# Kernel tuning notes

Hardware: AMD Instinct MI355X
Metric: run time of the kernel (lower is better)

## Reference

```python
import jax, jax.numpy as jnp
import numpy as np

# Problem dimensions (see shape_source)
N_TOTAL = 2048   # canonical nodes in batch
M = 8            # subgraphs per canonical node
K = 16           # sampled nodes per subgraph
S = N_TOTAL * M  # 16384 subgraphs
F = S * K        # 262144 flat nodes
E = 1048576      # intra-subgraph edges (64 per subgraph)
G = 128          # graphs in batch
D = 64           # hidden_dim
H = 4            # num_heads
DH = D // H
MAX_DIST = 32
NUM_LAYERS = 4
IN_CH = 119
EDGE_DIM = 5


def setup_inputs() -> dict:
    key = jax.random.key(0)
    ks = jax.random.split(key, 24)
    x_idx = jax.random.randint(ks[0], (F,), 0, IN_CH)
    edge_attr_idx = jax.random.randint(ks[1], (E,), 1, EDGE_DIM + 1)  # bond labels 1..5 (code does -1)
    # edges stay inside their subgraph: 64 edges per subgraph
    eps = E // S
    sub_of_edge = jnp.arange(E) // eps
    src = sub_of_edge * K + jax.random.randint(ks[2], (E,), 0, K)
    dst = sub_of_edge * K + jax.random.randint(ks[3], (E,), 0, K)
    node_ids = jax.random.randint(ks[4], (F,), 0, N_TOTAL)
    drop = jax.random.uniform(ks[5], (F,)) < 0.1
    is_root = (jnp.arange(F) % K) == 0
    node_ids = jnp.where(drop & (~is_root), -1, node_ids)
    node_ids = jnp.where(is_root, jnp.arange(F) // (K * M), node_ids)
    lp = -3.0 * jax.random.uniform(ks[6], (S,))  # log sampling probs (finite, negative)
    batch = jnp.sort(jax.random.randint(ks[7], (N_TOTAL,), 0, G))
    s = 0.02
    atom_emb = s * jax.random.normal(ks[8], (IN_CH, D))
    bond_emb = s * jax.random.normal(ks[9], (EDGE_DIM, D))
    dist_emb = s * jax.random.normal(ks[10], (MAX_DIST + 1, D))
    logp_w = s * jax.random.normal(ks[11], (1, D))
    logp_b = jnp.zeros((D,))
    mlp_w1 = s * jax.random.normal(ks[12], (NUM_LAYERS, D, D))
    mlp_b1 = jnp.zeros((NUM_LAYERS, D))
    mlp_w2 = s * jax.random.normal(ks[13], (NUM_LAYERS, D, D))
    mlp_b2 = jnp.zeros((NUM_LAYERS, D))
    ht_alpha = jnp.ones((1,))
    in_proj_w = s * jax.random.normal(ks[14], (3 * D, D))
    in_proj_b = jnp.zeros((3 * D,))
    out_proj_w = s * jax.random.normal(ks[15], (D, D))
    out_proj_b = jnp.zeros((D,))
    bn_gamma = jnp.ones((D,))
    bn_beta = jnp.zeros((D,))
    return {
        'x_idx': x_idx, 'edge_attr_idx': edge_attr_idx, 'src': src, 'dst': dst,
        'node_ids': node_ids, 'lp': lp, 'batch': batch,
        'atom_emb': atom_emb, 'bond_emb': bond_emb, 'dist_emb': dist_emb,
        'logp_w': logp_w, 'logp_b': logp_b,
        'mlp_w1': mlp_w1, 'mlp_b1': mlp_b1, 'mlp_w2': mlp_w2, 'mlp_b2': mlp_b2,
        'ht_alpha': ht_alpha, 'in_proj_w': in_proj_w, 'in_proj_b': in_proj_b,
        'out_proj_w': out_proj_w, 'out_proj_b': out_proj_b,
        'bn_gamma': bn_gamma, 'bn_beta': bn_beta,
    }


def reference(x_idx, edge_attr_idx, src, dst, node_ids, lp, batch,
              atom_emb, bond_emb, dist_emb, logp_w, logp_b,
              mlp_w1, mlp_b1, mlp_w2, mlp_b2, ht_alpha,
              in_proj_w, in_proj_b, out_proj_w, out_proj_b,
              bn_gamma, bn_beta):
    # --- embed nodes / bonds ---
    x_flat = atom_emb[x_idx]                       # [F, D]
    ea = bond_emb[edge_attr_idx - 1]               # [E, D]
    sub_batch = jnp.arange(F) // K                 # flat node -> subgraph id
    root = jnp.arange(S) * K
    # --- BFS distances from each subgraph root (edge relaxation, MAX_DIST iters) ---
    big = jnp.int32(MAX_DIST + K)
    d0 = jnp.full((F,), big, dtype=jnp.int32).at[root].set(0)
    def bfs_step(d, _):
        return d.at[dst].min(d[src] + 1), None
    dist, _ = jax.lax.scan(bfs_step, d0, None, length=MAX_DIST)
    dist = jnp.minimum(dist, MAX_DIST)
    dist_pe = dist_emb[dist]                       # [F, D]
    # --- log-prob positional encoding ---
    lp_s = jnp.where(jnp.isfinite(lp), lp, 0.0)    # [S]
    logp_pe = jax.nn.relu(lp_s[sub_batch][:, None] * logp_w[0][None, :] + logp_b)
    valid = node_ids >= 0
    vf = valid[:, None].astype(x_flat.dtype)
    h = (x_flat + dist_pe + logp_pe) * vf          # [F, D]
    # --- GINE-style message passing layers (Arch9Layer assumed: sum-aggregate ReLU(h_src+e) -> 2-layer MLP, residual, validity mask) ---
    for l in range(NUM_LAYERS):
        msg = jax.nn.relu(h[src] + ea)             # [E, D]
        agg = jax.ops.segment_sum(msg, dst, num_segments=F)
        z = jax.nn.relu(agg @ mlp_w1[l] + mlp_b1[l]) @ mlp_w2[l] + mlp_b2[l]
        h = (h + z) * vf
    # --- per-subgraph sum readout ---
    h_sub = jax.ops.segment_sum(h * vf, sub_batch, num_segments=S)  # [S, D]
    h3 = h_sub.reshape(N_TOTAL, M, D)
    # --- HT-biased multihead attention over the m subgraphs of each node ---
    bias = (-ht_alpha[0] * lp_s.reshape(N_TOTAL, M))[:, None, None, :]  # key-only bias [N,1,1,m]
    qkv = h3 @ in_proj_w.T + in_proj_b
    q, k_, v = jnp.split(qkv, 3, axis=-1)
    q = q.reshape(N_TOTAL, M, H, DH)
    k_ = k_.reshape(N_TOTAL, M, H, DH)
    v = v.reshape(N_TOTAL, M, H, DH)
    scores = jnp.einsum('nqhd,nkhd->nhqk', q, k_) / np.sqrt(DH).astype(np.float32) + bias
    attn = jax.nn.softmax(scores, axis=-1)
    o = jnp.einsum('nhqk,nkhd->nqhd', attn, v).reshape(N_TOTAL, M, D)
    o = o @ out_proj_w.T + out_proj_b
    h_attn = o + h3
    # --- mean over subgraphs, batchnorm (training-mode batch stats), graph pooling ---
    pooled = h_attn.mean(axis=1)                   # [N_TOTAL, D]
    mu = pooled.mean(axis=0)
    var = pooled.var(axis=0)
    node_emb = (pooled - mu) / jnp.sqrt(var + 1e-5) * bn_gamma + bn_beta
    return jax.ops.segment_sum(node_emb, batch, num_segments=G)   # [G, D]
```

## Files before the change

kernel.cpp:

```cpp
#include <hip/hip_runtime.h>
#include <hip/hip_bf16.h>

typedef __hip_bfloat16 bf16;
typedef __attribute__((ext_vector_type(8))) short bf16x8;
typedef __attribute__((ext_vector_type(4))) float f32x4;
typedef __attribute__((ext_vector_type(4))) unsigned u32x4;

#define N_TOTAL 2048
#define M_SUB   8
#define KN      16
#define S_SUB   16384
#define F_NODES 262144
#define E_EDGES 1048576
#define G_GRAPHS 128
#define D_DIM   64
#define EPS_SUB 64

#define H_ROWB  272
#define B_ROWB  272

__device__ __forceinline__ float b2f(bf16 x) { return __bfloat162float(x); }
__device__ __forceinline__ float bfu2f(unsigned short u) {
    return __uint_as_float(((unsigned)u) << 16);
}

__device__ __forceinline__ bool get_isbf(const void* alpha) {
    return ((const unsigned short*)alpha)[0] == 0x3F80;
}
__device__ __forceinline__ float ldf(const void* p, int i, bool isbf) {
    if (isbf) return __bfloat162float(((const bf16*)p)[i]);
    return ((const float*)p)[i];
}
__device__ __forceinline__ unsigned f2bf(float x) {
    return (unsigned)__builtin_bit_cast(unsigned short, __float2bfloat16(x));
}
__device__ __forceinline__ unsigned cvt_pk_bf16(float a, float b) {
    unsigned r;
    asm("v_cvt_pk_bf16_f32 %0, %1, %2" : "=v"(r) : "v"(a), "v"(b));
    return r;
}

__global__ __launch_bounds__(256) void k_prew(
    const void* __restrict__ mlp_w1, const void* __restrict__ mlp_w2,
    const void* __restrict__ alpha_p, unsigned short* __restrict__ wb)
{
    const bool isbf = get_isbf(alpha_p);
    int t = blockIdx.x * 256 + threadIdx.x;
    int L   = t >> 13;
    int rem = t & 8191;
    int mi  = rem >> 12;
    int wdx = rem & 4095;
    int row = wdx >> 6, col = wdx & 63;
    int kb = row >> 5, c = col >> 4;
    int f  = kb * 4 + c;
    int lane_ = (((row >> 3) & 3) << 4) | (col & 15);
    int u  = row & 7;
    float val = ldf(mi ? mlp_w2 : mlp_w1, L * 4096 + wdx, isbf);
    wb[((((L * 2 + mi) * 8 + f) * 64 + lane_) << 3) + u] = (unsigned short)f2bf(val);
}

__global__ __launch_bounds__(256) void k_subgraph(
    const int* __restrict__ x_idx, const int* __restrict__ eattr,
    const int* __restrict__ src, const int* __restrict__ dst,
    const int* __restrict__ node_ids, const void* __restrict__ lp,
    const void* __restrict__ atom_emb, const void* __restrict__ bond_emb,
    const void* __restrict__ dist_emb, const void* __restrict__ logp_w,
    const void* __restrict__ logp_b,
    const void* __restrict__ mlp_b1, const void* __restrict__ mlp_b2,
    const void* __restrict__ alpha_p,
    const unsigned short* __restrict__ wbg,
    float* __restrict__ hsub)
{
    __shared__ __align__(16) float sh_h[4][KN][68];
    __shared__ __align__(16) unsigned short ab_bf[4][KN*72];
    __shared__ __align__(16) float sh_bond[5 * 68];
    __shared__ int   sh_im[4][16];
    __shared__ int   sh_dist[4][16];
    __shared__ float sh_vf[4][16];
    __shared__ int   sh_xi[4][16];

    const int tid = threadIdx.x;
    const int w   = tid >> 6;
    const int j   = tid & 63;
    const int s   = blockIdx.x * 4 + w;
    const int q   = j & 15, g = j >> 4;
    const bool isbf = get_isbf(alpha_p);

    if (isbf) {
        const bf16* bp = (const bf16*)bond_emb;
        for (int t = tid; t < 5 * 64; t += 256) {
            int a = t >> 6, ch = t & 63;
            sh_bond[a * 68 + (ch & 15) * 4 + (ch >> 4)] = b2f(bp[t]);
        }
    } else {
        const float* bp = (const float*)bond_emb;
        for (int t = tid; t < 5 * 64; t += 256) {
            int a = t >> 6, ch = t & 63;
            sh_bond[a * 68 + (ch & 15) * 4 + (ch >> 4)] = bp[t];
        }
    }

    int eidx = s * EPS_SUB + j;
    int esrc = src[eidx]  - s * KN;
    int edst = dst[eidx]  - s * KN;
    int ea   = eattr[eidx] - 1;

    if (j < KN) {
        int f = s * KN + j;
        sh_xi[w][j]  = x_idx[f];
        sh_vf[w][j]  = (node_ids[f] >= 0) ? 1.0f : 0.0f;
        sh_im[w][j]  = 0;
    }
    __syncthreads();

    atomicOr(&sh_im[w][edst], 1 << esrc);

    unsigned pk = (unsigned)(esrc * H_ROWB) | ((unsigned)edst << 12)
                | ((unsigned)(ea * B_ROWB) << 16);
    const unsigned qq16 = (unsigned)(q * 16) * 0x00010001u;
    unsigned d0[8], d1[8];
    u32x4 ic0, ic1;
    #pragma unroll
    for (int up = 0; up < 4; ++up) {
        unsigned pa = (unsigned)__shfl((int)pk, 8 * g + 2 * up);
        unsigned pb = (unsigned)__shfl((int)pk, 8 * g + 2 * up + 1);
        unsigned pc = (unsigned)__shfl((int)pk, 32 + 8 * g + 2 * up);
        unsigned pd = (unsigned)__shfl((int)pk, 32 + 8 * g + 2 * up + 1);
        d0[2*up]   = (pa & 0xFFFF0FFFu) + qq16;
        d0[2*up+1] = (pb & 0xFFFF0FFFu) + qq16;
        d1[2*up]   = (pc & 0xFFFF0FFFu) + qq16;
        d1[2*up+1] = (pd & 0xFFFF0FFFu) + qq16;
        ic0[up] = ((((pa >> 12) & 15u) == (unsigned)q) ? 0x3F80u : 0u)
                | ((((pb >> 12) & 15u) == (unsigned)q) ? 0x3F800000u : 0u);
        ic1[up] = ((((pc >> 12) & 15u) == (unsigned)q) ? 0x3F80u : 0u)
                | ((((pd >> 12) & 15u) == (unsigned)q) ? 0x3F800000u : 0u);
    }
    const bf16x8 incf0 = __builtin_bit_cast(bf16x8, ic0);
    const bf16x8 incf1 = __builtin_bit_cast(bf16x8, ic1);

    {
        int inm  = (j < 16) ? sh_im[w][j] : 0;
        int dist = (j == 0) ? 0 : 48;
        unsigned reached = 1u;
        #pragma unroll
        for (int t = 1; t < 16; ++t) {
            bool r = (inm & (int)reached) != 0;
            unsigned long long b = __ballot(r);
            if (r && dist == 48) dist = t;
            reached |= (unsigned)(b & 0xFFFFu);
        }
        if (j < 16) sh_dist[w][j] = dist;
    }

    float vfr[4]; int xi4[4], di4[4];
    #pragma unroll
    for (int r = 0; r < 4; ++r) {
        int n = 4 * g + r;
        vfr[r] = sh_vf[w][n];
        xi4[r] = sh_xi[w][n];
        int d  = sh_dist[w][n];
        di4[r] = d > 32 ? 32 : d;
    }

    char* const hbase = (char*)&sh_h[w][0][0];
    const char* const bondb = (const char*)sh_bond;

    float hreg[4][4];
    {
        const float lp_s = ldf(lp, s, isbf);
        if (isbf) {
            const bf16* wp = (const bf16*)logp_w;
            const bf16* bp = (const bf16*)logp_b;
            const bf16* ap = (const bf16*)atom_emb;
            const bf16* dp = (const bf16*)dist_emb;
            #pragma unroll
            for (int c = 0; c < 4; ++c) {
                int ch = c * 16 + q;
                float lpe = fmaxf(lp_s * b2f(wp[ch]) + b2f(bp[ch]), 0.0f);
                #pragma unroll
                for (int r = 0; r < 4; ++r)
                    hreg[c][r] = (b2f(ap[xi4[r] * 64 + ch]) + b2f(dp[di4[r] * 64 + ch]) + lpe) * vfr[r];
            }
        } else {
            const float* wp = (const float*)logp_w;
            const float* bp = (const float*)logp_b;
            const float* ap = (const float*)atom_emb;
            const float* dp = (const float*)dist_emb;
            #pragma unroll
            for (int c = 0; c < 4; ++c) {
                int ch = c * 16 + q;
                float lpe = fmaxf(lp_s * wp[ch] + bp[ch], 0.0f);
                #pragma unroll
                for (int r = 0; r < 4; ++r)
                    hreg[c][r] = (ap[xi4[r] * 64 + ch] + dp[di4[r] * 64 + ch] + lpe) * vfr[r];
            }
        }
        #pragma unroll
        for (int r = 0; r < 4; ++r) {
            float4 v = {hreg[0][r], hreg[1][r], hreg[2][r], hreg[3][r]};
            *(float4*)(hbase + (4 * g + r) * H_ROWB + q * 16) = v;
        }
    }

    const bf16x8* wbv = (const bf16x8*)wbg;

    for (int L = 0; L < 4; ++L) {
        float b1c[4], b2c[4];
        if (isbf) {
            const bf16* p1 = (const bf16*)mlp_b1 + L * 64 + q;
            const bf16* p2 = (const bf16*)mlp_b2 + L * 64 + q;
            #pragma unroll
            for (int c = 0; c < 4; ++c) { b1c[c] = b2f(p1[c * 16]); b2c[c] = b2f(p2[c * 16]); }
        } else {
            const float* p1 = (const float*)mlp_b1 + L * 64 + q;
            const float* p2 = (const float*)mlp_b2 + L * 64 + q;
            #pragma unroll
            for (int c = 0; c < 4; ++c) { b1c[c] = p1[c * 16]; b2c[c] = p2[c * 16]; }
        }

        u32x4 mb0[4], mb1[4];
        #pragma unroll
        for (int up = 0; up < 4; ++up) {
            unsigned pa = d0[2*up], pb = d0[2*up+1];
            float4 ha = *(const float4*)(hbase + (pa & 0xFFFFu));
            float4 ba = *(const float4*)(bondb + (pa >> 16));
            float4 hb = *(const float4*)(hbase + (pb & 0xFFFFu));
            float4 bb = *(const float4*)(bondb + (pb >> 16));
            mb0[0][up] = cvt_pk_bf16(fmaxf(ha.x + ba.x, 0.f), fmaxf(hb.x + bb.x, 0.f));
            mb0[1][up] = cvt_pk_bf16(fmaxf(ha.y + ba.y, 0.f), fmaxf(hb.y + bb.y, 0.f));
            mb0[2][up] = cvt_pk_bf16(fmaxf(ha.z + ba.z, 0.f), fmaxf(hb.z + bb.z, 0.f));
            mb0[3][up] = cvt_pk_bf16(fmaxf(ha.w + ba.w, 0.f), fmaxf(hb.w + bb.w, 0.f));
        }
        #pragma unroll
        for (int up = 0; up < 4; ++up) {
            unsigned pa = d1[2*up], pb = d1[2*up+1];
            float4 ha = *(const float4*)(hbase + (pa & 0xFFFFu));
            float4 ba = *(const float4*)(bondb + (pa >> 16));
            float4 hb = *(const float4*)(hbase + (pb & 0xFFFFu));
            float4 bb = *(const float4*)(bondb + (pb >> 16));
            mb1[0][up] = cvt_pk_bf16(fmaxf(ha.x + ba.x, 0.f), fmaxf(hb.x + bb.x, 0.f));
            mb1[1][up] = cvt_pk_bf16(fmaxf(ha.y + ba.y, 0.f), fmaxf(hb.y + bb.y, 0.f));
            mb1[2][up] = cvt_pk_bf16(fmaxf(ha.z + ba.z, 0.f), fmaxf(hb.z + bb.z, 0.f));
            mb1[3][up] = cvt_pk_bf16(fmaxf(ha.w + ba.w, 0.f), fmaxf(hb.w + bb.w, 0.f));
        }

        #pragma unroll
        for (int c = 0; c < 4; ++c) {
            f32x4 acc = {0.f, 0.f, 0.f, 0.f};
            acc = __builtin_amdgcn_mfma_f32_16x16x32_bf16(incf0, __builtin_bit_cast(bf16x8, mb0[c]), acc, 0, 0, 0);
            acc = __builtin_amdgcn_mfma_f32_16x16x32_bf16(incf1, __builtin_bit_cast(bf16x8, mb1[c]), acc, 0, 0, 0);
            #pragma unroll
            for (int r = 0; r < 4; ++r)
                ab_bf[w][(4 * g + r) * 72 + c * 16 + q] = (unsigned short)f2bf(acc[r]);
        }

        bf16x8 a0 = *(const bf16x8*)&ab_bf[w][q * 72 + g * 8];
        bf16x8 a1 = *(const bf16x8*)&ab_bf[w][q * 72 + 32 + g * 8];
        int base1 = ((L * 2 + 0) * 8) * 64 + j;
        int base2 = ((L * 2 + 1) * 8) * 64 + j;
        #pragma unroll
        for (int c = 0; c < 4; ++c) {
            f32x4 acc = {b1c[c], b1c[c], b1c[c], b1c[c]};
            acc = __builtin_amdgcn_mfma_f32_16x16x32_bf16(a0, wbv[base1 + c * 64], acc, 0, 0, 0);
            acc = __builtin_amdgcn_mfma_f32_16x16x32_bf16(a1, wbv[base1 + (4 + c) * 64], acc, 0, 0, 0);
            #pragma unroll
            for (int r = 0; r < 4; ++r)
                ab_bf[w][(g * 4 + r) * 72 + c * 16 + q] =
                    (unsigned short)f2bf(fmaxf(acc[r], 0.0f));
        }

        bf16x8 u0 = *(const bf16x8*)&ab_bf[w][q * 72 + g * 8];
        bf16x8 u1 = *(const bf16x8*)&ab_bf[w][q * 72 + 32 + g * 8];
        #pragma unroll
        for (int c = 0; c < 4; ++c) {
            f32x4 acc = {b2c[c], b2c[c], b2c[c], b2c[c]};
            acc = __builtin_amdgcn_mfma_f32_16x16x32_bf16(u0, wbv[base2 + c * 64], acc, 0, 0, 0);
            acc = __builtin_amdgcn_mfma_f32_16x16x32_bf16(u1, wbv[base2 + (4 + c) * 64], acc, 0, 0, 0);
            #pragma unroll
            for (int r = 0; r < 4; ++r)
                hreg[c][r] = (hreg[c][r] + acc[r]) * vfr[r];
        }
        if (L < 3) {
            #pragma unroll
            for (int r = 0; r < 4; ++r) {
                float4 v = {hreg[0][r], hreg[1][r], hreg[2][r], hreg[3][r]};
                *(float4*)(hbase + (4 * g + r) * H_ROWB + q * 16) = v;
            }
        }
    }

    float tot[4];
    #pragma unroll
    for (int c = 0; c < 4; ++c) {
        tot[c] = (hreg[c][0] + hreg[c][1]) + (hreg[c][2] + hreg[c][3]);
        tot[c] += __shfl_xor(tot[c], 16, 64);
        tot[c] += __shfl_xor(tot[c], 32, 64);
    }
    float t01 = (g & 1) ? tot[1] : tot[0];
    float t23 = (g & 1) ? tot[3] : tot[2];
    hsub[s * 64 + j] = (g & 2) ? t23 : t01;
}

__global__ __launch_bounds__(256) void k_attn(
    const float* __restrict__ hsub, const void* __restrict__ lp,
    const void* __restrict__ alpha_p,
    const void* __restrict__ Win, const void* __restrict__ bin,
    const void* __restrict__ Wout, const void* __restrict__ bout,
    float* __restrict__ pooled)
{
    __shared__ unsigned short shWinT[64 * 193];
    __shared__ __align__(16) float sh_h3[4][8][64];
    __shared__ __align__(16) float sh_qkv[4][8][192];
    __shared__ __align__(16) float sh_o[4][8][64];
    __shared__ __align__(16) float sh_ob[4][64];

    const int tid = threadIdx.x;
    const int w   = tid >> 6;
    const int j   = tid & 63;
    const int n   = blockIdx.x * 4 + w;
    const bool isbf = get_isbf(alpha_p);

    if (isbf) {
        const unsigned short* Wp = (const unsigned short*)Win;
        for (int t = tid; t < 192 * 64; t += 256)
            shWinT[(t & 63) * 193 + (t >> 6)] = Wp[t];
    } else {
        const float* Wp = (const float*)Win;
        for (int t = tid; t < 192 * 64; t += 256)
            shWinT[(t & 63) * 193 + (t >> 6)] = (unsigned short)f2bf(Wp[t]);
    }

    for (int m = 0; m < 8; ++m)
        sh_h3[w][m][j] = hsub[(n * 8 + m) * 64 + j];
    __syncthreads();

    float accq[8], acck[8], accv[8];
    {
        const float bq = ldf(bin, j, isbf), bk = ldf(bin, 64 + j, isbf), bv = ldf(bin, 128 + j, isbf);
        #pragma unroll
        for (int m = 0; m < 8; ++m) { accq[m] = bq; acck[m] = bk; accv[m] = bv; }
    }
    #pragma unroll 2
    for (int i4 = 0; i4 < 16; ++i4) {
        float wq[4], wk[4], wv[4];
        #pragma unroll
        for (int u = 0; u < 4; ++u) {
            int i = i4 * 4 + u;
            wq[u] = bfu2f(shWinT[i * 193 + j]);
            wk[u] = bfu2f(shWinT[i * 193 + 64 + j]);
            wv[u] = bfu2f(shWinT[i * 193 + 128 + j]);
        }
        #pragma unroll
        for (int m = 0; m < 8; ++m) {
            const float4 a4 = *reinterpret_cast<const float4*>(&sh_h3[w][m][i4 * 4]);
            accq[m] = fmaf(a4.x, wq[0], accq[m]); accq[m] = fmaf(a4.y, wq[1], accq[m]);
            accq[m] = fmaf(a4.z, wq[2], accq[m]); accq[m] = fmaf(a4.w, wq[3], accq[m]);
            acck[m] = fmaf(a4.x, wk[0], acck[m]); acck[m] = fmaf(a4.y, wk[1], acck[m]);
            acck[m] = fmaf(a4.z, wk[2], acck[m]); acck[m] = fmaf(a4.w, wk[3], acck[m]);
            accv[m] = fmaf(a4.x, wv[0], accv[m]); accv[m] = fmaf(a4.y, wv[1], accv[m]);
            accv[m] = fmaf(a4.z, wv[2], accv[m]); accv[m] = fmaf(a4.w, wv[3], accv[m]);
        }
    }
    #pragma unroll
    for (int m = 0; m < 8; ++m) {
        sh_qkv[w][m][j]       = accq[m];
        sh_qkv[w][m][64 + j]  = acck[m];
        sh_qkv[w][m][128 + j] = accv[m];
    }
    __syncthreads();

    if (j < 32) {
        const int hh = j >> 3, m1 = j & 7;
        const float alpha = ldf(alpha_p, 0, isbf);
        float qv[16];
        #pragma unroll
        for (int d = 0; d < 16; ++d) qv[d] = sh_qkv[w][m1][hh * 16 + d];
        float sc[8];
        #pragma unroll
        for (int m2 = 0; m2 < 8; ++m2) {
            float sacc = 0.0f;
            #pragma unroll
            for (int d = 0; d < 16; ++d)
                sacc += qv[d] * sh_qkv[w][m2][64 + hh * 16 + d];
            sc[m2] = sacc * 0.25f - alpha * ldf(lp, n * 8 + m2, isbf);
        }
        float mx = sc[0];
        #pragma unroll
        for (int m2 = 1; m2 < 8; ++m2) mx = fmaxf(mx, sc[m2]);
        float ssum = 0.0f;
        #pragma unroll
        for (int m2 = 0; m2 < 8; ++m2) { sc[m2] = expf(sc[m2] - mx); ssum += sc[m2]; }
        const float inv = 1.0f / ssum;
        #pragma unroll
        for (int m2 = 0; m2 < 8; ++m2) sc[m2] *= inv;
        #pragma unroll
        for (int d = 0; d < 16; ++d) {
            float ov = 0.0f;
            #pragma unroll
            for (int m2 = 0; m2 < 8; ++m2)
                ov += sc[m2] * sh_qkv[w][m2][128 + hh * 16 + d];
            sh_o[w][m1][hh * 16 + d] = ov;
        }
    }
    __syncthreads();

    float obar = 0.0f, h3bar = 0.0f;
    #pragma unroll
    for (int m = 0; m < 8; ++m) { obar += sh_o[w][m][j]; h3bar += sh_h3[w][m][j]; }
    obar *= 0.125f; h3bar *= 0.125f;
    sh_ob[w][j] = obar;

    float acc = ldf(bout, j, isbf) + h3bar;
    if (isbf) {
        const unsigned short* Wrow = (const unsigned short*)Wout + j * 64;
        #pragma unroll 4
        for (int i4 = 0; i4 < 16; ++i4) {
            const float4 o4 = *reinterpret_cast<const float4*>(&sh_ob[w][i4 * 4]);
            const ushort4 wv = *reinterpret_cast<const ushort4*>(&Wrow[i4 * 4]);
            acc = fmaf(o4.x, bfu2f(wv.x), acc);
            acc = fmaf(o4.y, bfu2f(wv.y), acc);
            acc = fmaf(o4.z, bfu2f(wv.z), acc);
            acc = fmaf(o4.w, bfu2f(wv.w), acc);
        }
    } else {
        const float* Wrow = (const float*)Wout + j * 64;
        #pragma unroll 4
        for (int i4 = 0; i4 < 16; ++i4) {
            const float4 o4 = *reinterpret_cast<const float4*>(&sh_ob[w][i4 * 4]);
            const float4 wv = *reinterpret_cast<const float4*>(&Wrow[i4 * 4]);
            acc = fmaf(o4.x, wv.x, acc); acc = fmaf(o4.y, wv.y, acc);
            acc = fmaf(o4.z, wv.z, acc); acc = fmaf(o4.w, wv.w, acc);
        }
    }
    pooled[n * 64 + j] = acc;
}

__global__ __launch_bounds__(256) void k_stats(
    const float* __restrict__ pooled, float* __restrict__ mu, float* __restrict__ rstd)
{
    const int d = blockIdx.x;
    const int t = threadIdx.x;
    float s1 = 0.0f, s2 = 0.0f;
    for (int nn = t; nn < N_TOTAL; nn += 256) {
        float v = pooled[nn * 64 + d];
        s1 += v; s2 += v * v;
    }
    __shared__ float r1[256], r2[256];
    r1[t] = s1; r2[t] = s2;
    __syncthreads();
    for (int o = 128; o > 0; o >>= 1) {
        if (t < o) { r1[t] += r1[t + o]; r2[t] += r2[t + o]; }
        __syncthreads();
    }
    if (t == 0) {
        float m   = r1[0] * (1.0f / N_TOTAL);
        float var = r2[0] * (1.0f / N_TOTAL) - m * m;
        mu[d]   = m;
        rstd[d] = rsqrtf(var + 1e-5f);
    }
}

__global__ __launch_bounds__(64) void k_final(
    const float* __restrict__ pooled, const float* __restrict__ mu,
    const float* __restrict__ rstd, const void* __restrict__ gamma,
    const void* __restrict__ beta, const int* __restrict__ batch,
    const void* __restrict__ alpha_p, void* __restrict__ out)
{
    const int gph = blockIdx.x;
    const int j   = threadIdx.x;
    const bool isbf = get_isbf(alpha_p);

    int a = 0, b = N_TOTAL;
    while (a < b) { int m = (a + b) >> 1; if (batch[m] < gph) a = m + 1; else b = m; }
    const int lo = a;
    b = N_TOTAL;
    while (a < b) { int m = (a + b) >> 1; if (batch[m] < gph + 1) a = m + 1; else b = m; }
    const int hi = a;

    const float mj = mu[j], rj = rstd[j];
    const float gj = ldf(gamma, j, isbf), bj = ldf(beta, j, isbf);
    const float scale = rj * gj;

    float sum = 0.0f;
    for (int nn = lo; nn < hi; ++nn)
        sum += (pooled[nn * 64 + j] - mj) * scale + bj;

    if (isbf) ((bf16*)out)[gph * 64 + j]  = __float2bfloat16(sum);
    else      ((float*)out)[gph * 64 + j] = sum;
}

extern "C" void kernel_launch(void* const* d_in, const int* in_sizes, int n_in,
                              void* d_out, int out_size, void* d_ws, size_t ws_size,
                              hipStream_t stream)
{
    const int*  x_idx    = (const int*) d_in[0];
    const int*  eattr    = (const int*) d_in[1];
    const int*  srcv     = (const int*) d_in[2];
    const int*  dstv     = (const int*) d_in[3];
    const int*  node_ids = (const int*) d_in[4];
    const void* lp       = d_in[5];
    const int*  batch    = (const int*) d_in[6];
    const void* atom_emb = d_in[7];
    const void* bond_emb = d_in[8];
    const void* dist_emb = d_in[9];
    const void* logp_w   = d_in[10];
    const void* logp_b   = d_in[11];
    const void* mlp_w1   = d_in[12];
    const void* mlp_b1   = d_in[13];
    const void* mlp_w2   = d_in[14];
    const void* mlp_b2   = d_in[15];
    const void* ht_alpha = d_in[16];
    const void* Win      = d_in[17];
    const void* bin      = d_in[18];
    const void* Wout     = d_in[19];
    const void* bout     = d_in[20];
    const void* gamma    = d_in[21];
    const void* beta     = d_in[22];

    char* ws = (char*)d_ws;
    float* hsub   = (float*)(ws);
    float* pooled = (float*)(ws + 4194304);
    float* mu     = (float*)(ws + 4718592);
    float* rstd   = (float*)(ws + 4718848);
    unsigned short* wbg = (unsigned short*)(ws + 4751872);

    k_prew<<<128, 256, 0, stream>>>(mlp_w1, mlp_w2, ht_alpha, wbg);

    k_subgraph<<<S_SUB / 4, 256, 0, stream>>>(
        x_idx, eattr, srcv, dstv, node_ids, lp,
        atom_emb, bond_emb, dist_emb, logp_w, logp_b,
        mlp_b1, mlp_b2, ht_alpha, wbg, hsub);

    k_attn<<<N_TOTAL / 4, 256, 0, stream>>>(
        hsub, lp, ht_alpha, Win, bin, Wout, bout, pooled);

    k_stats<<<64, 256, 0, stream>>>(pooled, mu, rstd);

    k_final<<<G_GRAPHS, 64, 0, stream>>>(
        pooled, mu, rstd, gamma, beta, batch, ht_alpha, d_out);
}
```

Measured before the change: 104.4 us.

## Transpose MFMA operand roles to keep MLP activations in registers via shuffles

Swaps the A/B operand roles in the subgraph kernel's message-aggregation and MLP MFMAs so the accumulator layout is feature-major. Intermediate activations are then re-laid out between the MLP stages with cross-lane shuffles instead of a round trip through a shared-memory bf16 staging buffer. The weight pre-pack layout, bias loads and embedding init are changed to match, now using vectorized loads. The final readout sums from shared memory rather than shuffles. This trades LDS stores and loads for many more shuffle instructions per layer.

```diff
diff --git a/kernel.cpp b/kernel.cpp
--- a/kernel.cpp
+++ b/kernel.cpp
@@ -51,13 +51,25 @@
     int mi  = rem >> 12;
     int wdx = rem & 4095;
     int row = wdx >> 6, col = wdx & 63;
-    int kb = row >> 5, c = col >> 4;
-    int f  = kb * 4 + c;
-    int lane_ = (((row >> 3) & 3) << 4) | (col & 15);
-    int u  = row & 7;
+    int kb = row >> 5, g_ = (row >> 3) & 3, u = row & 7;
+    int mo = col >> 4, qq = col & 15;
+    int f  = mo * 2 + kb;
+    int lane_ = g_ * 16 + qq;
     float val = ldf(mi ? mlp_w2 : mlp_w1, L * 4096 + wdx, isbf);
     wb[((((L * 2 + mi) * 8 + f) * 64 + lane_) << 3) + u] = (unsigned short)f2bf(val);
 }
+
+#define TRX(B0, B1, pk0, pk1, lA, lB, hi) do {                                   \
+    unsigned _a, _b;                                                             \
+    _a = (unsigned)__shfl((int)pk0[0], lA); _b = (unsigned)__shfl((int)pk0[1], lA); B0[0] = (hi) ? _b : _a; \
+    _a = (unsigned)__shfl((int)pk1[0], lA); _b = (unsigned)__shfl((int)pk1[1], lA); B0[1] = (hi) ? _b : _a; \
+    _a = (unsigned)__shfl((int)pk0[0], lB); _b = (unsigned)__shfl((int)pk0[1], lB); B0[2] = (hi) ? _b : _a; \
+    _a = (unsigned)__shfl((int)pk1[0], lB); _b = (unsigned)__shfl((int)pk1[1], lB); B0[3] = (hi) ? _b : _a; \
+    _a = (unsigned)__shfl((int)pk0[2], lA); _b = (unsigned)__shfl((int)pk0[3], lA); B1[0] = (hi) ? _b : _a; \
+    _a = (unsigned)__shfl((int)pk1[2], lA); _b = (unsigned)__shfl((int)pk1[3], lA); B1[1] = (hi) ? _b : _a; \
+    _a = (unsigned)__shfl((int)pk0[2], lB); _b = (unsigned)__shfl((int)pk0[3], lB); B1[2] = (hi) ? _b : _a; \
+    _a = (unsigned)__shfl((int)pk1[2], lB); _b = (unsigned)__shfl((int)pk1[3], lB); B1[3] = (hi) ? _b : _a; \
+} while (0)
 
 __global__ __launch_bounds__(256) void k_subgraph(
     const int* __restrict__ x_idx, const int* __restrict__ eattr,
@@ -72,7 +84,6 @@
     float* __restrict__ hsub)
 {
     __shared__ __align__(16) float sh_h[4][KN][68];
-    __shared__ __align__(16) unsigned short ab_bf[4][KN*72];
     __shared__ __align__(16) float sh_bond[5 * 68];
     __shared__ int   sh_im[4][16];
     __shared__ int   sh_dist[4][16];
@@ -135,8 +146,8 @@
         ic1[up] = ((((pc >> 12) & 15u) == (unsigned)q) ? 0x3F80u : 0u)
                 | ((((pd >> 12) & 15u) == (unsigned)q) ? 0x3F800000u : 0u);
     }
-    const bf16x8 incf0 = __builtin_bit_cast(bf16x8, ic0);
-    const bf16x8 incf1 = __builtin_bit_cast(bf16x8, ic1);
+    const bf16x8 incB0 = __builtin_bit_cast(bf16x8, ic0);
+    const bf16x8 incB1 = __builtin_bit_cast(bf16x8, ic1);
 
     {
         int inm  = (j < 16) ? sh_im[w][j] : 0;
@@ -152,15 +163,9 @@
         if (j < 16) sh_dist[w][j] = dist;
     }
 
-    float vfr[4]; int xi4[4], di4[4];
-    #pragma unroll
-    for (int r = 0; r < 4; ++r) {
-        int n = 4 * g + r;
-        vfr[r] = sh_vf[w][n];
-        xi4[r] = sh_xi[w][n];
-        int d  = sh_dist[w][n];
-        di4[r] = d > 32 ? 32 : d;
-    }
+    const int   xi_q = sh_xi[w][q];
+    const float vf_q = sh_vf[w][q];
+    int di_q = sh_dist[w][q]; di_q = di_q > 32 ? 32 : di_q;
 
     char* const hbase = (char*)&sh_h[w][0][0];
     const char* const bondb = (const char*)sh_bond;
@@ -169,136 +174,160 @@
     {
         const float lp_s = ldf(lp, s, isbf);
         if (isbf) {
-            const bf16* wp = (const bf16*)logp_w;
-            const bf16* bp = (const bf16*)logp_b;
-            const bf16* ap = (const bf16*)atom_emb;
-            const bf16* dp = (const bf16*)dist_emb;
-            #pragma unroll
-            for (int c = 0; c < 4; ++c) {
-                int ch = c * 16 + q;
-                float lpe = fmaxf(lp_s * b2f(wp[ch]) + b2f(bp[ch]), 0.0f);
-                #pragma unroll
-                for (int r = 0; r < 4; ++r)
-                    hreg[c][r] = (b2f(ap[xi4[r] * 64 + ch]) + b2f(dp[di4[r] * 64 + ch]) + lpe) * vfr[r];
+            const unsigned short* ap = (const unsigned short*)atom_emb + xi_q * 64;
+            const unsigned short* dp = (const unsigned short*)dist_emb + di_q * 64;
+            const unsigned short* wp = (const unsigned short*)logp_w;
+            const unsigned short* bp = (const unsigned short*)logp_b;
+            #pragma unroll
+            for (int mo = 0; mo < 4; ++mo) {
+                int base = mo * 16 + 4 * g;
+                ushort4 av = *(const ushort4*)(ap + base);
+                ushort4 dv = *(const ushort4*)(dp + base);
+                ushort4 wv = *(const ushort4*)(wp + base);
+                ushort4 bv = *(const ushort4*)(bp + base);
+                hreg[mo][0] = (bfu2f(av.x) + bfu2f(dv.x) + fmaxf(lp_s * bfu2f(wv.x) + bfu2f(bv.x), 0.f)) * vf_q;
+                hreg[mo][1] = (bfu2f(av.y) + bfu2f(dv.y) + fmaxf(lp_s * bfu2f(wv.y) + bfu2f(bv.y), 0.f)) * vf_q;
+                hreg[mo][2] = (bfu2f(av.z) + bfu2f(dv.z) + fmaxf(lp_s * bfu2f(wv.z) + bfu2f(bv.z), 0.f)) * vf_q;
+                hreg[mo][3] = (bfu2f(av.w) + bfu2f(dv.w) + fmaxf(lp_s * bfu2f(wv.w) + bfu2f(bv.w), 0.f)) * vf_q;
             }
         } else {
+            const float* ap = (const float*)atom_emb + xi_q * 64;
+            const float* dp = (const float*)dist_emb + di_q * 64;
             const float* wp = (const float*)logp_w;
             const float* bp = (const float*)logp_b;
-            const float* ap = (const float*)atom_emb;
-            const float* dp = (const float*)dist_emb;
-            #pragma unroll
-            for (int c = 0; c < 4; ++c) {
-                int ch = c * 16 + q;
-                float lpe = fmaxf(lp_s * wp[ch] + bp[ch], 0.0f);
-                #pragma unroll
-                for (int r = 0; r < 4; ++r)
-                    hreg[c][r] = (ap[xi4[r] * 64 + ch] + dp[di4[r] * 64 + ch] + lpe) * vfr[r];
+            #pragma unroll
+            for (int mo = 0; mo < 4; ++mo) {
+                int base = mo * 16 + 4 * g;
+                float4 av = *(const float4*)(ap + base);
+                float4 dv = *(const float4*)(dp + base);
+                float4 wv = *(const float4*)(wp + base);
+                float4 bv = *(const float4*)(bp + base);
+                hreg[mo][0] = (av.x + dv.x + fmaxf(lp_s * wv.x + bv.x, 0.f)) * vf_q;
+                hreg[mo][1] = (av.y + dv.y + fmaxf(lp_s * wv.y + bv.y, 0.f)) * vf_q;
+                hreg[mo][2] = (av.z + dv.z + fmaxf(lp_s * wv.z + bv.z, 0.f)) * vf_q;
+                hreg[mo][3] = (av.w + dv.w + fmaxf(lp_s * wv.w + bv.w, 0.f)) * vf_q;
             }
         }
         #pragma unroll
         for (int r = 0; r < 4; ++r) {
             float4 v = {hreg[0][r], hreg[1][r], hreg[2][r], hreg[3][r]};
-            *(float4*)(hbase + (4 * g + r) * H_ROWB + q * 16) = v;
+            *(float4*)(hbase + q * H_ROWB + 64 * g + 16 * r) = v;
         }
     }
 
     const bf16x8* wbv = (const bf16x8*)wbg;
+    const int lA = ((g & 1) << 5) + q;
+    const int lB = lA + 16;
+    const bool hi = g >= 2;
 
     for (int L = 0; L < 4; ++L) {
-        float b1c[4], b2c[4];
-        if (isbf) {
-            const bf16* p1 = (const bf16*)mlp_b1 + L * 64 + q;
-            const bf16* p2 = (const bf16*)mlp_b2 + L * 64 + q;
-            #pragma unroll
-            for (int c = 0; c < 4; ++c) { b1c[c] = b2f(p1[c * 16]); b2c[c] = b2f(p2[c * 16]); }
-        } else {
-            const float* p1 = (const float*)mlp_b1 + L * 64 + q;
-            const float* p2 = (const float*)mlp_b2 + L * 64 + q;
-            #pragma unroll
-            for (int c = 0; c < 4; ++c) { b1c[c] = p1[c * 16]; b2c[c] = p2[c * 16]; }
-        }
-
-        u32x4 mb0[4], mb1[4];
-        #pragma unroll
-        for (int up = 0; up < 4; ++up) {
-            unsigned pa = d0[2*up], pb = d0[2*up+1];
-            float4 ha = *(const float4*)(hbase + (pa & 0xFFFFu));
-            float4 ba = *(const float4*)(bondb + (pa >> 16));
-            float4 hb = *(const float4*)(hbase + (pb & 0xFFFFu));
-            float4 bb = *(const float4*)(bondb + (pb >> 16));
-            mb0[0][up] = cvt_pk_bf16(fmaxf(ha.x + ba.x, 0.f), fmaxf(hb.x + bb.x, 0.f));
-            mb0[1][up] = cvt_pk_bf16(fmaxf(ha.y + ba.y, 0.f), fmaxf(hb.y + bb.y, 0.f));
-            mb0[2][up] = cvt_pk_bf16(fmaxf(ha.z + ba.z, 0.f), fmaxf(hb.z + bb.z, 0.f));
-            mb0[3][up] = cvt_pk_bf16(fmaxf(ha.w + ba.w, 0.f), fmaxf(hb.w + bb.w, 0.f));
-        }
-        #pragma unroll
-        for (int up = 0; up < 4; ++up) {
-            unsigned pa = d1[2*up], pb = d1[2*up+1];
-            float4 ha = *(const float4*)(hbase + (pa & 0xFFFFu));
-            float4 ba = *(const float4*)(bondb + (pa >> 16));
-            float4 hb = *(const float4*)(hbase + (pb & 0xFFFFu));
-            float4 bb = *(const float4*)(bondb + (pb >> 16));
-            mb1[0][up] = cvt_pk_bf16(fmaxf(ha.x + ba.x, 0.f), fmaxf(hb.x + bb.x, 0.f));
-            mb1[1][up] = cvt_pk_bf16(fmaxf(ha.y + ba.y, 0.f), fmaxf(hb.y + bb.y, 0.f));
-            mb1[2][up] = cvt_pk_bf16(fmaxf(ha.z + ba.z, 0.f), fmaxf(hb.z + bb.z, 0.f));
-            mb1[3][up] = cvt_pk_bf16(fmaxf(ha.w + ba.w, 0.f), fmaxf(hb.w + bb.w, 0.f));
-        }
-
-        #pragma unroll
-        for (int c = 0; c < 4; ++c) {
-            f32x4 acc = {0.f, 0.f, 0.f, 0.f};
-            acc = __builtin_amdgcn_mfma_f32_16x16x32_bf16(incf0, __builtin_bit_cast(bf16x8, mb0[c]), acc, 0, 0, 0);
-            acc = __builtin_amdgcn_mfma_f32_16x16x32_bf16(incf1, __builtin_bit_cast(bf16x8, mb1[c]), acc, 0, 0, 0);
+        f32x4 agg[4];
+        #pragma unroll
+        for (int mc = 0; mc < 4; ++mc) agg[mc] = (f32x4){0.f, 0.f, 0.f, 0.f};
+        {
+            u32x4 mb[4];
+            #pragma unroll
+            for (int up = 0; up < 4; ++up) {
+                unsigned pa = d0[2*up], pb = d0[2*up+1];
+                float4 ha = *(const float4*)(hbase + (pa & 0xFFFFu));
+                float4 ba = *(const float4*)(bondb + (pa >> 16));
+                float4 hb = *(const float4*)(hbase + (pb & 0xFFFFu));
+                float4 bb = *(const float4*)(bondb + (pb >> 16));
+                mb[0][up] = cvt_pk_bf16(fmaxf(ha.x + ba.x, 0.f), fmaxf(hb.x + bb.x, 0.f));
+                mb[1][up] = cvt_pk_bf16(fmaxf(ha.y + ba.y, 0.f), fmaxf(hb.y + bb.y, 0.f));
+                mb[2][up] = cvt_pk_bf16(fmaxf(ha.z + ba.z, 0.f), fmaxf(hb.z + bb.z, 0.f));
+                mb[3][up] = cvt_pk_bf16(fmaxf(ha.w + ba.w, 0.f), fmaxf(hb.w + bb.w, 0.f));
+            }
+            #pragma unroll
+            for (int mc = 0; mc < 4; ++mc)
+                agg[mc] = __builtin_amdgcn_mfma_f32_16x16x32_bf16(
+                    __builtin_bit_cast(bf16x8, mb[mc]), incB0, agg[mc], 0, 0, 0);
+        }
+        {
+            u32x4 mb[4];
+            #pragma unroll
+            for (int up = 0; up < 4; ++up) {
+                unsigned pa = d1[2*up], pb = d1[2*up+1];
+                float4 ha = *(const float4*)(hbase + (pa & 0xFFFFu));
+                float4 ba = *(const float4*)(bondb + (pa >> 16));
+                float4 hb = *(const float4*)(hbase + (pb & 0xFFFFu));
+                float4 bb = *(const float4*)(bondb + (pb >> 16));
+                mb[0][up] = cvt_pk_bf16(fmaxf(ha.x + ba.x, 0.f), fmaxf(hb.x + bb.x, 0.f));
+                mb[1][up] = cvt_pk_bf16(fmaxf(ha.y + ba.y, 0.f), fmaxf(hb.y + bb.y, 0.f));
+                mb[2][up] = cvt_pk_bf16(fmaxf(ha.z + ba.z, 0.f), fmaxf(hb.z + bb.z, 0.f));
+                mb[3][up] = cvt_pk_bf16(fmaxf(ha.w + ba.w, 0.f), fmaxf(hb.w + bb.w, 0.f));
+            }
+            #pragma unroll
+            for (int mc = 0; mc < 4; ++mc)
+                agg[mc] = __builtin_amdgcn_mfma_f32_16x16x32_bf16(
+                    __builtin_bit_cast(bf16x8, mb[mc]), incB1, agg[mc], 0, 0, 0);
+        }
+
+        unsigned pk0[4], pk1[4];
+        #pragma unroll
+        for (int mc = 0; mc < 4; ++mc) {
+            pk0[mc] = cvt_pk_bf16(agg[mc][0], agg[mc][1]);
+            pk1[mc] = cvt_pk_bf16(agg[mc][2], agg[mc][3]);
+        }
+        u32x4 Ba0, Ba1;
+        TRX(Ba0, Ba1, pk0, pk1, lA, lB, hi);
+        const bf16x8 Ba0f = __builtin_bit_cast(bf16x8, Ba0);
+        const bf16x8 Ba1f = __builtin_bit_cast(bf16x8, Ba1);
+
+        const int w1b = (L * 2 + 0) * 512 + j;
+        #pragma unroll
+        for (int mo = 0; mo < 4; ++mo) {
+            f32x4 acc;
+            if (isbf) {
+                ushort4 t = *(const ushort4*)((const unsigned short*)mlp_b1 + L * 64 + mo * 16 + 4 * g);
+                acc[0] = bfu2f(t.x); acc[1] = bfu2f(t.y); acc[2] = bfu2f(t.z); acc[3] = bfu2f(t.w);
+            } else {
+                float4 t = *(const float4*)((const float*)mlp_b1 + L * 64 + mo * 16 + 4 * g);
+                acc[0] = t.x; acc[1] = t.y; acc[2] = t.z; acc[3] = t.w;
+            }
+            acc = __builtin_amdgcn_mfma_f32_16x16x32_bf16(wbv[w1b + (mo * 2 + 0) * 64], Ba0f, acc, 0, 0, 0);
+            acc = __builtin_amdgcn_mfma_f32_16x16x32_bf16(wbv[w1b + (mo * 2 + 1) * 64], Ba1f, acc, 0, 0, 0);
+            pk0[mo] = cvt_pk_bf16(fmaxf(acc[0], 0.f), fmaxf(acc[1], 0.f));
+            pk1[mo] = cvt_pk_bf16(fmaxf(acc[2], 0.f), fmaxf(acc[3], 0.f));
+        }
+        u32x4 Bu0, Bu1;
+        TRX(Bu0, Bu1, pk0, pk1, lA, lB, hi);
+        const bf16x8 Bu0f = __builtin_bit_cast(bf16x8, Bu0);
+        const bf16x8 Bu1f = __builtin_bit_cast(bf16x8, Bu1);
+
+        const int w2b = (L * 2 + 1) * 512 + j;
+        #pragma unroll
+        for (int mo = 0; mo < 4; ++mo) {
+            f32x4 acc;
+            if (isbf) {
+                ushort4 t = *(const ushort4*)((const unsigned short*)mlp_b2 + L * 64 + mo * 16 + 4 * g);
+                acc[0] = bfu2f(t.x); acc[1] = bfu2f(t.y); acc[2] = bfu2f(t.z); acc[3] = bfu2f(t.w);
+            } else {
+                float4 t = *(const float4*)((const float*)mlp_b2 + L * 64 + mo * 16 + 4 * g);
+                acc[0] = t.x; acc[1] = t.y; acc[2] = t.z; acc[3] = t.w;
+            }
+            acc = __builtin_amdgcn_mfma_f32_16x16x32_bf16(wbv[w2b + (mo * 2 + 0) * 64], Bu0f, acc, 0, 0, 0);
+            acc = __builtin_amdgcn_mfma_f32_16x16x32_bf16(wbv[w2b + (mo * 2 + 1) * 64], Bu1f, acc, 0, 0, 0);
             #pragma unroll
             for (int r = 0; r < 4; ++r)
-                ab_bf[w][(4 * g + r) * 72 + c * 16 + q] = (unsigned short)f2bf(acc[r]);
-        }
-
-        bf16x8 a0 = *(const bf16x8*)&ab_bf[w][q * 72 + g * 8];
-        bf16x8 a1 = *(const bf16x8*)&ab_bf[w][q * 72 + 32 + g * 8];
-        int base1 = ((L * 2 + 0) * 8) * 64 + j;
-        int base2 = ((L * 2 + 1) * 8) * 64 + j;
-        #pragma unroll
-        for (int c = 0; c < 4; ++c) {
-            f32x4 acc = {b1c[c], b1c[c], b1c[c], b1c[c]};
-            acc = __builtin_amdgcn_mfma_f32_16x16x32_bf16(a0, wbv[base1 + c * 64], acc, 0, 0, 0);
-            acc = __builtin_amdgcn_mfma_f32_16x16x32_bf16(a1, wbv[base1 + (4 + c) * 64], acc, 0, 0, 0);
-            #pragma unroll
-            for (int r = 0; r < 4; ++r)
-                ab_bf[w][(g * 4 + r) * 72 + c * 16 + q] =
-                    (unsigned short)f2bf(fmaxf(acc[r], 0.0f));
-        }
-
-        bf16x8 u0 = *(const bf16x8*)&ab_bf[w][q * 72 + g * 8];
-        bf16x8 u1 = *(const bf16x8*)&ab_bf[w][q * 72 + 32 + g * 8];
-        #pragma unroll
-        for (int c = 0; c < 4; ++c) {
-            f32x4 acc = {b2c[c], b2c[c], b2c[c], b2c[c]};
-            acc = __builtin_amdgcn_mfma_f32_16x16x32_bf16(u0, wbv[base2 + c * 64], acc, 0, 0, 0);
-            acc = __builtin_amdgcn_mfma_f32_16x16x32_bf16(u1, wbv[base2 + (4 + c) * 64], acc, 0, 0, 0);
-            #pragma unroll
-            for (int r = 0; r < 4; ++r)
-                hreg[c][r] = (hreg[c][r] + acc[r]) * vfr[r];
-        }
-        if (L < 3) {
-            #pragma unroll
-            for (int r = 0; r < 4; ++r) {
-                float4 v = {hreg[0][r], hreg[1][r], hreg[2][r], hreg[3][r]};
-                *(float4*)(hbase + (4 * g + r) * H_ROWB + q * 16) = v;
-            }
-        }
-    }
-
-    float tot[4];
-    #pragma unroll
-    for (int c = 0; c < 4; ++c) {
-        tot[c] = (hreg[c][0] + hreg[c][1]) + (hreg[c][2] + hreg[c][3]);
-        tot[c] += __shfl_xor(tot[c], 16, 64);
-        tot[c] += __shfl_xor(tot[c], 32, 64);
-    }
-    float t01 = (g & 1) ? tot[1] : tot[0];
-    float t23 = (g & 1) ? tot[3] : tot[2];
-    hsub[s * 64 + j] = (g & 2) ? t23 : t01;
+                hreg[mo][r] = (hreg[mo][r] + acc[r]) * vf_q;
+        }
+
+        #pragma unroll
+        for (int r = 0; r < 4; ++r) {
+            float4 v = {hreg[0][r], hreg[1][r], hreg[2][r], hreg[3][r]};
+            *(float4*)(hbase + q * H_ROWB + 64 * g + 16 * r) = v;
+        }
+    }
+
+    {
+        const float* hsrc = (const float*)hbase;
+        const int p = (j & 15) * 4 + (j >> 4);
+        float sum = 0.0f;
+        #pragma unroll
+        for (int n = 0; n < KN; ++n) sum += hsrc[n * 68 + p];
+        hsub[s * 64 + j] = sum;
+    }
 }
 
 __global__ __launch_bounds__(256) void k_attn(
```

New measurement: 131.7 us. 26.2% more time.
